# Performance work log

Measured on AMD Instinct MI355X. Metric: run time of the kernel, lower is better.

The kernel has to match this reference:

```python
import jax, jax.numpy as jnp
import numpy as np

B, T, H, D, V = 16, 64, 512, 512, 50257


def setup_inputs() -> dict:
    key = jax.random.key(0)
    ks = jax.random.split(key, 12)
    s = 0.05
    return {
        "sentiment_hidden": jax.random.normal(ks[0], (B, H), jnp.float32),
        "other_hidden": jax.random.normal(ks[1], (B, H), jnp.float32),
        "targets": jax.random.randint(ks[2], (B, T), 0, V),
        # SpaceTransformer: Linear(2H -> H) + ReLU (dropout inactive in eval)
        "Wc": jax.random.normal(ks[3], (H, 2 * H), jnp.float32) * s,
        "bc": jnp.zeros((H,), jnp.float32),
        # embedding table [V, D]
        "E": jax.random.normal(ks[4], (V, D), jnp.float32) * s,
        # LSTM params, PyTorch gate order (i, f, g, o)
        "W_ih": jax.random.normal(ks[5], (4 * H, D), jnp.float32) * s,
        "W_hh": jax.random.normal(ks[6], (4 * H, H), jnp.float32) * s,
        "b_ih": jnp.zeros((4 * H,), jnp.float32),
        "b_hh": jnp.zeros((4 * H,), jnp.float32),
        # output projection [V, H]
        "Wo": jax.random.normal(ks[7], (V, H), jnp.float32) * s,
        "bo": jnp.zeros((V,), jnp.float32),
    }


def reference(sentiment_hidden, other_hidden, targets, Wc, bc, E, W_ih, W_hh, b_ih, b_hh, Wo, bo):
    # combine: SpaceTransformer(Linear(2H->H) + ReLU)
    inputs = jax.nn.relu(jnp.concatenate([sentiment_hidden, other_hidden], axis=-1) @ Wc.T + bc)
    new_representation = inputs            # [B, H]
    bsz = inputs.shape[0]
    # teacher forcing: step 0 uses BOS token id 1, step t>0 uses targets[:, t-1]
    tokens = jnp.concatenate([jnp.ones((bsz, 1), targets.dtype), targets[:, :-1]], axis=1)  # [B, T]
    emb = E[tokens]                        # [B, T, D]
    # precompute input contribution to all gates: [B, T, 4H]
    xg = jnp.einsum("btd,gd->btg", emb, W_ih) + b_ih + b_hh

    def step(carry, x_t):                  # x_t: [B, 4H]
        h, c = carry
        g = x_t + h @ W_hh.T
        i, f, gg, o = jnp.split(g, 4, axis=-1)
        c = jax.nn.sigmoid(f) * c + jax.nn.sigmoid(i) * jnp.tanh(gg)
        h = jax.nn.sigmoid(o) * jnp.tanh(c)
        return (h, c), h

    c0 = jnp.zeros_like(inputs)
    (_, _), hs = jax.lax.scan(step, (inputs, c0), jnp.swapaxes(xg, 0, 1))
    hs = jnp.swapaxes(hs, 0, 1)            # [B, T, H]
    logits = jnp.einsum("bth,vh->btv", hs, Wo) + bo   # [B, T, V]
    predictions = jnp.argmax(logits, axis=-1)          # [B, T]
    return logits, predictions, new_representation
```

## Files before the change

kernel.cpp:

```cpp
#include <hip/hip_runtime.h>
#include <cstdint>
#include <cstddef>

typedef unsigned short u16;
typedef unsigned int   u32;
typedef unsigned long long u64;

typedef __attribute__((ext_vector_type(8))) short short8;
typedef __attribute__((ext_vector_type(4))) float f32x4;

#define NB_B 16
#define NT   64
#define NH   512
#define ND   512
#define NV   50257
#define NG   2048
#define LSTM_NBLK 32
#define UPB  16

__device__ __forceinline__ u16 f2bf(float f) {
    u32 u = __builtin_bit_cast(u32, f);
    return (u16)((u + 0x7FFFu + ((u >> 16) & 1u)) >> 16);
}
__device__ __forceinline__ float bf2f(u16 h) {
    return __builtin_bit_cast(float, (u32)h << 16);
}
__device__ __forceinline__ float sigm(float x) { return 1.0f / (1.0f + expf(-x)); }

__global__ void k_prep(const float* __restrict__ Whh, u16* __restrict__ Whi,
                       u16* __restrict__ Wlo, u64* __restrict__ argm,
                       u32* __restrict__ cnt) {
    int i = blockIdx.x * 256 + threadIdx.x;
    if (i < NG * NH) {
        float f = Whh[i];
        u16 hi = f2bf(f);
        Whi[i] = hi;
        Wlo[i] = f2bf(f - bf2f(hi));
    }
    if (i < NB_B * NT) argm[i] = 0ull;
    if (i < NT) cnt[i] = 0u;
}

__global__ __launch_bounds__(256) void k_combine(
    const float* __restrict__ sh, const float* __restrict__ oh,
    const float* __restrict__ Wc, const float* __restrict__ bc,
    float* __restrict__ h0, float* __restrict__ rep_out) {
    __shared__ float x[1024];
    int b = blockIdx.x, tid = threadIdx.x;
    for (int i = tid; i < 1024; i += 256)
        x[i] = (i < NH) ? sh[b * NH + i] : oh[b * NH + i - NH];
    __syncthreads();
    for (int n = tid; n < NH; n += 256) {
        const float* wr = Wc + (size_t)n * 1024;
        float s = 0.f;
        #pragma unroll 4
        for (int k = 0; k < 1024; k += 4) {
            float4 w = *(const float4*)(wr + k);
            s += x[k] * w.x + x[k+1] * w.y + x[k+2] * w.z + x[k+3] * w.w;
        }
        s += bc[n];
        s = fmaxf(s, 0.f);
        h0[b * NH + n] = s;
        rep_out[b * NH + n] = s;
    }
}

__global__ void k_gather(const int* __restrict__ targets, const float* __restrict__ E,
                         float* __restrict__ emb) {
    int bt = blockIdx.x;
    int b = bt >> 6, t = bt & 63;
    int tok = (t == 0) ? 1 : targets[b * NT + t - 1];
    const float4* s = (const float4*)(E + (size_t)tok * ND);
    float4* d = (float4*)(emb + (size_t)bt * ND);
    d[threadIdx.x] = s[threadIdx.x];
}

template<bool ARGMAX>
__global__ __launch_bounds__(256, 2) void k_gemm(
    const float* __restrict__ A,
    const float* __restrict__ Bm,
    const float* __restrict__ bias1,
    const float* __restrict__ bias2,
    float* __restrict__ C,
    u64* __restrict__ argm,
    int M, int N, int K, int NB) {
    __shared__ u16 sAh[128 * 64], sAl[128 * 64], sBh[128 * 64], sBl[128 * 64];
    int tid = threadIdx.x, lane = tid & 63, w = tid >> 6;
    int wm = w >> 1, wn = w & 1;

    int bid = blockIdx.x;
    int full = NB >> 3;
    int thresh = full << 6;
    int m_idx, n_idx;
    if (bid < thresh) {
        int g = bid >> 6, r = bid & 63;
        n_idx = g * 8 + (r & 7);
        m_idx = r >> 3;
    } else {
        int r2 = bid - thresh;
        int nrem = NB - (full << 3);
        n_idx = (full << 3) + r2 % nrem;
        m_idx = r2 / nrem;
    }
    int mbase = m_idx * 128, nbase = n_idx * 128;

    f32x4 acc[4][4];
    #pragma unroll
    for (int i = 0; i < 4; ++i)
        #pragma unroll
        for (int j = 0; j < 4; ++j) acc[i][j] = (f32x4){0.f, 0.f, 0.f, 0.f};

    const int lc = lane & 15, lk4 = lane >> 4;

    #pragma unroll 1
    for (int kc = 0; kc < K; kc += 64) {
        #pragma unroll
        for (int it = 0; it < 4; ++it) {
            int gi = tid + it * 256;
            int row = gi >> 3, gin = gi & 7;
            int gs8 = ((gin ^ (row & 7)) << 3);
            {
                const float* src = A + (size_t)(mbase + row) * K + kc + gin * 8;
                float4 f0 = *(const float4*)(src);
                float4 f1 = *(const float4*)(src + 4);
                float fv[8] = {f0.x, f0.y, f0.z, f0.w, f1.x, f1.y, f1.z, f1.w};
                short8 h8, l8;
                #pragma unroll
                for (int e = 0; e < 8; ++e) {
                    u16 hi = f2bf(fv[e]);
                    h8[e] = (short)hi;
                    l8[e] = (short)f2bf(fv[e] - bf2f(hi));
                }
                *(short8*)&sAh[row * 64 + gs8] = h8;
                *(short8*)&sAl[row * 64 + gs8] = l8;
            }
            {
                int n = nbase + row;
                short8 h8, l8;
                if (n < N) {
                    const float* src = Bm + (size_t)n * K + kc + gin * 8;
                    float4 f0 = *(const float4*)(src);
                    float4 f1 = *(const float4*)(src + 4);
                    float fv[8] = {f0.x, f0.y, f0.z, f0.w, f1.x, f1.y, f1.z, f1.w};
                    #pragma unroll
                    for (int e = 0; e < 8; ++e) {
                        u16 hi = f2bf(fv[e]);
                        h8[e] = (short)hi;
                        l8[e] = (short)f2bf(fv[e] - bf2f(hi));
                    }
                } else {
                    #pragma unroll
                    for (int e = 0; e < 8; ++e) { h8[e] = 0; l8[e] = 0; }
                }
                *(short8*)&sBh[row * 64 + gs8] = h8;
                *(short8*)&sBl[row * 64 + gs8] = l8;
            }
        }
        __syncthreads();
        #pragma unroll
        for (int ks = 0; ks < 2; ++ks) {
            short8 ah[4], al[4], bh[4], bl[4];
            #pragma unroll
            for (int mi = 0; mi < 4; ++mi) {
                int r = wm * 64 + mi * 16 + lc;
                int gs8 = (((ks * 4 + lk4) ^ (r & 7)) << 3);
                ah[mi] = *(const short8*)&sAh[r * 64 + gs8];
                al[mi] = *(const short8*)&sAl[r * 64 + gs8];
            }
            #pragma unroll
            for (int ni = 0; ni < 4; ++ni) {
                int r = wn * 64 + ni * 16 + lc;
                int gs8 = (((ks * 4 + lk4) ^ (r & 7)) << 3);
                bh[ni] = *(const short8*)&sBh[r * 64 + gs8];
                bl[ni] = *(const short8*)&sBl[r * 64 + gs8];
            }
            #pragma unroll
            for (int mi = 0; mi < 4; ++mi)
                #pragma unroll
                for (int ni = 0; ni < 4; ++ni) {
                    acc[mi][ni] = __builtin_amdgcn_mfma_f32_16x16x32_bf16(ah[mi], bh[ni], acc[mi][ni], 0, 0, 0);
                    acc[mi][ni] = __builtin_amdgcn_mfma_f32_16x16x32_bf16(al[mi], bh[ni], acc[mi][ni], 0, 0, 0);
                    acc[mi][ni] = __builtin_amdgcn_mfma_f32_16x16x32_bf16(ah[mi], bl[ni], acc[mi][ni], 0, 0, 0);
                }
        }
        __syncthreads();
    }

    float bsum[4];
    int cols[4];
    #pragma unroll
    for (int ni = 0; ni < 4; ++ni) {
        int col = nbase + wn * 64 + ni * 16 + lc;
        cols[ni] = col;
        float bv = 0.f;
        if (col < N) { bv = bias1[col]; if (bias2) bv += bias2[col]; }
        bsum[ni] = bv;
    }
    #pragma unroll
    for (int mi = 0; mi < 4; ++mi) {
        #pragma unroll
        for (int r_ = 0; r_ < 4; ++r_) {
            int row = mbase + wm * 64 + mi * 16 + (lk4 << 2) + r_;
            float* crow = C + (size_t)row * N;
            u64 best = 0ull;
            #pragma unroll
            for (int ni = 0; ni < 4; ++ni) {
                if (cols[ni] < N) {
                    float v = acc[mi][ni][r_] + bsum[ni];
                    crow[cols[ni]] = v;
                    if (ARGMAX) {
                        u32 bits = __builtin_bit_cast(u32, v);
                        u32 mono = (bits & 0x80000000u) ? ~bits : (bits | 0x80000000u);
                        u64 p = ((u64)mono << 32) | (u64)(0xFFFFFFFFu - (u32)cols[ni]);
                        best = best > p ? best : p;
                    }
                }
            }
            if (ARGMAX) {
                #pragma unroll
                for (int s = 1; s < 16; s <<= 1) {
                    u64 o = __shfl_xor((unsigned long long)best, s, 64);
                    best = best > o ? best : o;
                }
                if (lc == 0) atomicMax(&argm[row], best);
            }
        }
    }
}

__global__ __launch_bounds__(256, 1) void k_lstm(
    const float* __restrict__ xg, const float* __restrict__ h0,
    const u16* __restrict__ Whi, const u16* __restrict__ Wlo,
    float* __restrict__ hs,
    u32* __restrict__ Ghi, u32* __restrict__ Glo,
    u32* __restrict__ cnt) {
    __shared__ u16 hhi[16 * 512];
    __shared__ u16 hlo[16 * 512];
    __shared__ float g_lds[4 * 256];

    const int tid = threadIdx.x;
    const int lane = tid & 63, w = tid >> 6;
    const int blk = blockIdx.x;
    const int u0 = blk * UPB;
    const int lc = lane & 15, lk4 = lane >> 4;
    const int bown = tid >> 4, uown = tid & 15;

    short8 bh[16], bl[16];
    {
        size_t base = (size_t)(w * NH + u0 + lc) * NH + lk4 * 8;
        #pragma unroll
        for (int kk = 0; kk < 16; ++kk) {
            bh[kk] = *(const short8*)(Whi + base + kk * 32);
            bl[kk] = *(const short8*)(Wlo + base + kk * 32);
        }
    }

    #pragma unroll
    for (int i = 0; i < 32; ++i) {
        int idx = i * 256 + tid;
        int b = idx >> 9, k = idx & 511;
        float f = h0[b * NH + k];
        u16 hi = f2bf(f), lo = f2bf(f - bf2f(hi));
        int g = k >> 3;
        int ea = b * 512 + ((g ^ (b & 7)) << 3) + (k & 7);
        hhi[ea] = hi;
        hlo[ea] = lo;
    }
    float c = 0.f;
    __syncthreads();

    #pragma unroll 1
    for (int t = 0; t < NT; ++t) {
        f32x4 a0 = (f32x4){0.f,0.f,0.f,0.f};
        f32x4 a1 = (f32x4){0.f,0.f,0.f,0.f};
        f32x4 a2 = (f32x4){0.f,0.f,0.f,0.f};
        #pragma unroll
        for (int kk = 0; kk < 16; ++kk) {
            int g = kk * 4 + lk4;
            int ea = lc * 512 + ((g ^ (lc & 7)) << 3);
            short8 ah = *(const short8*)&hhi[ea];
            short8 al = *(const short8*)&hlo[ea];
            a0 = __builtin_amdgcn_mfma_f32_16x16x32_bf16(ah, bh[kk], a0, 0, 0, 0);
            a1 = __builtin_amdgcn_mfma_f32_16x16x32_bf16(al, bh[kk], a1, 0, 0, 0);
            a2 = __builtin_amdgcn_mfma_f32_16x16x32_bf16(ah, bl[kk], a2, 0, 0, 0);
        }
        #pragma unroll
        for (int r = 0; r < 4; ++r)
            g_lds[w * 256 + (lk4 * 4 + r) * 16 + lc] = a0[r] + a1[r] + a2[r];
        __syncthreads();

        const float* xrow = xg + (size_t)(bown * NT + t) * NG + u0 + uown;
        float gi = g_lds[0 * 256 + tid] + xrow[0];
        float gf = g_lds[1 * 256 + tid] + xrow[NH];
        float gg = g_lds[2 * 256 + tid] + xrow[2 * NH];
        float go = g_lds[3 * 256 + tid] + xrow[3 * NH];
        c = sigm(gf) * c + sigm(gi) * tanhf(gg);
        float h = sigm(go) * tanhf(c);
        hs[(size_t)(bown * NT + t) * NH + u0 + uown] = h;

        if (t < NT - 1) {
            u16 hi = f2bf(h), lo = f2bf(h - bf2f(hi));
            u32 ohi = (u32)(u16)__shfl_xor((int)(u32)hi, 1, 64);
            u32 olo = (u32)(u16)__shfl_xor((int)(u32)lo, 1, 64);
            int buf = (t & 1) * 4096;
            if ((tid & 1) == 0) {
                int word = bown * 256 + ((u0 + uown) >> 1);
                __hip_atomic_store(&Ghi[buf + word], (u32)hi | (ohi << 16),
                                   __ATOMIC_RELAXED, __HIP_MEMORY_SCOPE_AGENT);
                __hip_atomic_store(&Glo[buf + word], (u32)lo | (olo << 16),
                                   __ATOMIC_RELAXED, __HIP_MEMORY_SCOPE_AGENT);
            }
            __threadfence();
            __syncthreads();
            if (tid == 0) {
                __hip_atomic_fetch_add(&cnt[t], 1u, __ATOMIC_RELEASE, __HIP_MEMORY_SCOPE_AGENT);
                while (__hip_atomic_load(&cnt[t], __ATOMIC_ACQUIRE, __HIP_MEMORY_SCOPE_AGENT) < LSTM_NBLK) {}
            }
            __syncthreads();
            #pragma unroll
            for (int i = 0; i < 16; ++i) {
                int word = i * 256 + tid;
                int b = word >> 8, k2 = word & 255;
                u32 vh = __hip_atomic_load(&Ghi[buf + word], __ATOMIC_RELAXED, __HIP_MEMORY_SCOPE_AGENT);
                u32 vl = __hip_atomic_load(&Glo[buf + word], __ATOMIC_RELAXED, __HIP_MEMORY_SCOPE_AGENT);
                int k = k2 * 2, g = k >> 3;
                int ea = b * 512 + ((g ^ (b & 7)) << 3) + (k & 7);
                *(u32*)&hhi[ea] = vh;
                *(u32*)&hlo[ea] = vl;
            }
            __syncthreads();
        }
    }
}

__global__ void k_decode(const u64* __restrict__ argm, float* __restrict__ pred) {
    int i = blockIdx.x * 256 + threadIdx.x;
    if (i < NB_B * NT) {
        u32 enc = (u32)(argm[i] & 0xFFFFFFFFull);
        pred[i] = (float)(0xFFFFFFFFu - enc);
    }
}

extern "C" void kernel_launch(void* const* d_in, const int* in_sizes, int n_in,
                              void* d_out, int out_size, void* d_ws, size_t ws_size,
                              hipStream_t stream) {
    const float* sh  = (const float*)d_in[0];
    const float* oh  = (const float*)d_in[1];
    const int*   tg  = (const int*)d_in[2];
    const float* Wc  = (const float*)d_in[3];
    const float* bc  = (const float*)d_in[4];
    const float* E   = (const float*)d_in[5];
    const float* Wih = (const float*)d_in[6];
    const float* Whh = (const float*)d_in[7];
    const float* bih = (const float*)d_in[8];
    const float* bhh = (const float*)d_in[9];
    const float* Wo  = (const float*)d_in[10];
    const float* bo  = (const float*)d_in[11];

    float* out_logits = (float*)d_out;
    float* out_pred   = out_logits + (size_t)NB_B * NT * NV;
    float* out_rep    = out_pred + NB_B * NT;

    char* ws = (char*)d_ws;
    u16*   Whi  = (u16*)(ws);
    u16*   Wlo  = (u16*)(ws + (size_t)2  * 1024 * 1024);
    float* emb  = (float*)(ws + (size_t)4  * 1024 * 1024);
    float* xg   = (float*)(ws + (size_t)6  * 1024 * 1024);
    float* hs   = (float*)(ws + (size_t)14 * 1024 * 1024);
    float* h0   = (float*)(ws + (size_t)16 * 1024 * 1024);
    u64*   argm = (u64*)(ws + (size_t)16 * 1024 * 1024 + 32 * 1024);
    u32*   Ghi  = (u32*)(ws + (size_t)16 * 1024 * 1024 + 40 * 1024);
    u32*   Glo  = (u32*)(ws + (size_t)16 * 1024 * 1024 + 72 * 1024);
    u32*   cnt  = (u32*)(ws + (size_t)16 * 1024 * 1024 + 104 * 1024);

    k_prep<<<dim3(4096), dim3(256), 0, stream>>>(Whh, Whi, Wlo, argm, cnt);
    k_combine<<<dim3(NB_B), dim3(256), 0, stream>>>(sh, oh, Wc, bc, h0, out_rep);
    k_gather<<<dim3(NB_B * NT), dim3(128), 0, stream>>>(tg, E, emb);
    k_gemm<false><<<dim3(8 * 16), dim3(256), 0, stream>>>(
        emb, Wih, bih, bhh, xg, (u64*)nullptr, NB_B * NT, NG, ND, 16);
    k_lstm<<<dim3(LSTM_NBLK), dim3(256), 0, stream>>>(xg, h0, Whi, Wlo, hs, Ghi, Glo, cnt);
    k_gemm<true><<<dim3(8 * 393), dim3(256), 0, stream>>>(
        hs, Wo, bo, (const float*)nullptr, out_logits, argm, NB_B * NT, NV, NH, 393);
    k_decode<<<dim3(4), dim3(256), 0, stream>>>(argm, out_pred);
}
```

Baseline: 1.396 ms.

## Pre-pack Wo and hs as bf16 hi/lo pairs; per-block flag barrier in LSTM

Adds a packing pass that converts Wo once into interleaved bf16 hi/lo u32 words, so the logits GEMM tiles no longer re-split fp32 into bf16 pairs on every load (Wo is reloaded for each of the eight M tiles). The LSTM now writes packed hidden states directly, which the output GEMM consumes without conversion. The LSTM step barrier changes from a shared atomic counter with a spin by thread 0 to per-block flags polled by 32 lanes with sleep, and the hidden-state exchange uses a packed layout. The packed Wo buffer needs about 100 MB of workspace and an extra pass over Wo. The new barrier drops the explicit release fence and relies on vmcnt waits, so memory ordering is a risk.

```diff
diff --git a/kernel.cpp b/kernel.cpp
--- a/kernel.cpp
+++ b/kernel.cpp
@@ -1,4 +1,5 @@
 #include <hip/hip_runtime.h>
+#include <hip/hip_bf16.h>
 #include <cstdint>
 #include <cstddef>
 
@@ -19,8 +20,8 @@
 #define UPB  16
 
 __device__ __forceinline__ u16 f2bf(float f) {
-    u32 u = __builtin_bit_cast(u32, f);
-    return (u16)((u + 0x7FFFu + ((u >> 16) & 1u)) >> 16);
+    __hip_bfloat16 b = __float2bfloat16(f);
+    return __builtin_bit_cast(u16, b);
 }
 __device__ __forceinline__ float bf2f(u16 h) {
     return __builtin_bit_cast(float, (u32)h << 16);
@@ -29,7 +30,7 @@
 
 __global__ void k_prep(const float* __restrict__ Whh, u16* __restrict__ Whi,
                        u16* __restrict__ Wlo, u64* __restrict__ argm,
-                       u32* __restrict__ cnt) {
+                       u32* __restrict__ flags) {
     int i = blockIdx.x * 256 + threadIdx.x;
     if (i < NG * NH) {
         float f = Whh[i];
@@ -38,7 +39,24 @@
         Wlo[i] = f2bf(f - bf2f(hi));
     }
     if (i < NB_B * NT) argm[i] = 0ull;
-    if (i < NT) cnt[i] = 0u;
+    if (i < NT * LSTM_NBLK) flags[i] = 0u;
+}
+
+__global__ void k_pack_wo(const float* __restrict__ Wo, u32* __restrict__ Wo_pk) {
+    size_t base = ((size_t)blockIdx.x * 256 + threadIdx.x) * 8;
+    if (base >= (size_t)NV * NH) return;
+    float4 f0 = *(const float4*)(Wo + base);
+    float4 f1 = *(const float4*)(Wo + base + 4);
+    float fv[8] = {f0.x, f0.y, f0.z, f0.w, f1.x, f1.y, f1.z, f1.w};
+    u32 ov[8];
+    #pragma unroll
+    for (int e = 0; e < 8; ++e) {
+        u16 hi = f2bf(fv[e]);
+        u16 lo = f2bf(fv[e] - bf2f(hi));
+        ov[e] = ((u32)hi << 16) | (u32)lo;
+    }
+    *(uint4*)(Wo_pk + base) = (uint4){ov[0], ov[1], ov[2], ov[3]};
+    *(uint4*)(Wo_pk + base + 4) = (uint4){ov[4], ov[5], ov[6], ov[7]};
 }
 
 __global__ __launch_bounds__(256) void k_combine(
@@ -75,10 +93,10 @@
     d[threadIdx.x] = s[threadIdx.x];
 }
 
-template<bool ARGMAX>
+template<bool ARGMAX, bool APK, bool BPK>
 __global__ __launch_bounds__(256, 2) void k_gemm(
-    const float* __restrict__ A,
-    const float* __restrict__ Bm,
+    const void* __restrict__ Av,
+    const void* __restrict__ Bv,
     const float* __restrict__ bias1,
     const float* __restrict__ bias2,
     float* __restrict__ C,
@@ -120,25 +138,19 @@
             int row = gi >> 3, gin = gi & 7;
             int gs8 = ((gin ^ (row & 7)) << 3);
             {
-                const float* src = A + (size_t)(mbase + row) * K + kc + gin * 8;
-                float4 f0 = *(const float4*)(src);
-                float4 f1 = *(const float4*)(src + 4);
-                float fv[8] = {f0.x, f0.y, f0.z, f0.w, f1.x, f1.y, f1.z, f1.w};
                 short8 h8, l8;
-                #pragma unroll
-                for (int e = 0; e < 8; ++e) {
-                    u16 hi = f2bf(fv[e]);
-                    h8[e] = (short)hi;
-                    l8[e] = (short)f2bf(fv[e] - bf2f(hi));
-                }
-                *(short8*)&sAh[row * 64 + gs8] = h8;
-                *(short8*)&sAl[row * 64 + gs8] = l8;
-            }
-            {
-                int n = nbase + row;
-                short8 h8, l8;
-                if (n < N) {
-                    const float* src = Bm + (size_t)n * K + kc + gin * 8;
+                if (APK) {
+                    const u32* src = (const u32*)Av + (size_t)(mbase + row) * K + kc + gin * 8;
+                    uint4 p0 = *(const uint4*)(src);
+                    uint4 p1 = *(const uint4*)(src + 4);
+                    u32 pv[8] = {p0.x, p0.y, p0.z, p0.w, p1.x, p1.y, p1.z, p1.w};
+                    #pragma unroll
+                    for (int e = 0; e < 8; ++e) {
+                        h8[e] = (short)(u16)(pv[e] >> 16);
+                        l8[e] = (short)(u16)(pv[e] & 0xFFFFu);
+                    }
+                } else {
+                    const float* src = (const float*)Av + (size_t)(mbase + row) * K + kc + gin * 8;
                     float4 f0 = *(const float4*)(src);
                     float4 f1 = *(const float4*)(src + 4);
                     float fv[8] = {f0.x, f0.y, f0.z, f0.w, f1.x, f1.y, f1.z, f1.w};
@@ -147,6 +159,36 @@
                         u16 hi = f2bf(fv[e]);
                         h8[e] = (short)hi;
                         l8[e] = (short)f2bf(fv[e] - bf2f(hi));
+                    }
+                }
+                *(short8*)&sAh[row * 64 + gs8] = h8;
+                *(short8*)&sAl[row * 64 + gs8] = l8;
+            }
+            {
+                int n = nbase + row;
+                short8 h8, l8;
+                if (n < N) {
+                    if (BPK) {
+                        const u32* src = (const u32*)Bv + (size_t)n * K + kc + gin * 8;
+                        uint4 p0 = *(const uint4*)(src);
+                        uint4 p1 = *(const uint4*)(src + 4);
+                        u32 pv[8] = {p0.x, p0.y, p0.z, p0.w, p1.x, p1.y, p1.z, p1.w};
+                        #pragma unroll
+                        for (int e = 0; e < 8; ++e) {
+                            h8[e] = (short)(u16)(pv[e] >> 16);
+                            l8[e] = (short)(u16)(pv[e] & 0xFFFFu);
+                        }
+                    } else {
+                        const float* src = (const float*)Bv + (size_t)n * K + kc + gin * 8;
+                        float4 f0 = *(const float4*)(src);
+                        float4 f1 = *(const float4*)(src + 4);
+                        float fv[8] = {f0.x, f0.y, f0.z, f0.w, f1.x, f1.y, f1.z, f1.w};
+                        #pragma unroll
+                        for (int e = 0; e < 8; ++e) {
+                            u16 hi = f2bf(fv[e]);
+                            h8[e] = (short)hi;
+                            l8[e] = (short)f2bf(fv[e] - bf2f(hi));
+                        }
                     }
                 } else {
                     #pragma unroll
@@ -231,9 +273,9 @@
 __global__ __launch_bounds__(256, 1) void k_lstm(
     const float* __restrict__ xg, const float* __restrict__ h0,
     const u16* __restrict__ Whi, const u16* __restrict__ Wlo,
-    float* __restrict__ hs,
-    u32* __restrict__ Ghi, u32* __restrict__ Glo,
-    u32* __restrict__ cnt) {
+    u32* __restrict__ hs_pk,
+    u32* __restrict__ H,
+    u32* __restrict__ flags) {
     __shared__ u16 hhi[16 * 512];
     __shared__ u16 hlo[16 * 512];
     __shared__ float g_lds[4 * 256];
@@ -296,37 +338,42 @@
         float go = g_lds[3 * 256 + tid] + xrow[3 * NH];
         c = sigm(gf) * c + sigm(gi) * tanhf(gg);
         float h = sigm(go) * tanhf(c);
-        hs[(size_t)(bown * NT + t) * NH + u0 + uown] = h;
+        u16 hi = f2bf(h), lo = f2bf(h - bf2f(hi));
+        u32 pk = ((u32)hi << 16) | (u32)lo;
+        hs_pk[(size_t)(bown * NT + t) * NH + u0 + uown] = pk;
 
         if (t < NT - 1) {
-            u16 hi = f2bf(h), lo = f2bf(h - bf2f(hi));
-            u32 ohi = (u32)(u16)__shfl_xor((int)(u32)hi, 1, 64);
-            u32 olo = (u32)(u16)__shfl_xor((int)(u32)lo, 1, 64);
-            int buf = (t & 1) * 4096;
-            if ((tid & 1) == 0) {
-                int word = bown * 256 + ((u0 + uown) >> 1);
-                __hip_atomic_store(&Ghi[buf + word], (u32)hi | (ohi << 16),
+            const int buf = (t & 1) * 8192;
+            __hip_atomic_store(&H[buf + bown * NH + u0 + uown], pk,
+                               __ATOMIC_RELAXED, __HIP_MEMORY_SCOPE_AGENT);
+            asm volatile("s_waitcnt vmcnt(0)" ::: "memory");
+            __syncthreads();
+            if (tid == 0)
+                __hip_atomic_store(&flags[t * LSTM_NBLK + blk], 1u,
                                    __ATOMIC_RELAXED, __HIP_MEMORY_SCOPE_AGENT);
-                __hip_atomic_store(&Glo[buf + word], (u32)lo | (olo << 16),
-                                   __ATOMIC_RELAXED, __HIP_MEMORY_SCOPE_AGENT);
-            }
-            __threadfence();
-            __syncthreads();
-            if (tid == 0) {
-                __hip_atomic_fetch_add(&cnt[t], 1u, __ATOMIC_RELEASE, __HIP_MEMORY_SCOPE_AGENT);
-                while (__hip_atomic_load(&cnt[t], __ATOMIC_ACQUIRE, __HIP_MEMORY_SCOPE_AGENT) < LSTM_NBLK) {}
-            }
-            __syncthreads();
+            if (lane < LSTM_NBLK) {
+                while (__hip_atomic_load(&flags[t * LSTM_NBLK + lane],
+                                         __ATOMIC_RELAXED, __HIP_MEMORY_SCOPE_AGENT) == 0) {
+                    __builtin_amdgcn_s_sleep(1);
+                }
+            }
+            asm volatile("" ::: "memory");
             #pragma unroll
-            for (int i = 0; i < 16; ++i) {
-                int word = i * 256 + tid;
-                int b = word >> 8, k2 = word & 255;
-                u32 vh = __hip_atomic_load(&Ghi[buf + word], __ATOMIC_RELAXED, __HIP_MEMORY_SCOPE_AGENT);
-                u32 vl = __hip_atomic_load(&Glo[buf + word], __ATOMIC_RELAXED, __HIP_MEMORY_SCOPE_AGENT);
-                int k = k2 * 2, g = k >> 3;
-                int ea = b * 512 + ((g ^ (b & 7)) << 3) + (k & 7);
-                *(u32*)&hhi[ea] = vh;
-                *(u32*)&hlo[ea] = vl;
+            for (int i = 0; i < 4; ++i) {
+                int grp = i * 256 + tid;
+                int b = grp >> 6, gidx = grp & 63;
+                int ubase = gidx << 3;
+                short8 h8, l8;
+                #pragma unroll
+                for (int e = 0; e < 8; ++e) {
+                    u32 v = __hip_atomic_load(&H[buf + b * NH + ubase + e],
+                                              __ATOMIC_RELAXED, __HIP_MEMORY_SCOPE_AGENT);
+                    h8[e] = (short)(u16)(v >> 16);
+                    l8[e] = (short)(u16)(v & 0xFFFFu);
+                }
+                int ea = b * 512 + ((gidx ^ (b & 7)) << 3);
+                *(short8*)&hhi[ea] = h8;
+                *(short8*)&hlo[ea] = l8;
             }
             __syncthreads();
         }
@@ -362,24 +409,32 @@
     float* out_rep    = out_pred + NB_B * NT;
 
     char* ws = (char*)d_ws;
-    u16*   Whi  = (u16*)(ws);
-    u16*   Wlo  = (u16*)(ws + (size_t)2  * 1024 * 1024);
-    float* emb  = (float*)(ws + (size_t)4  * 1024 * 1024);
-    float* xg   = (float*)(ws + (size_t)6  * 1024 * 1024);
-    float* hs   = (float*)(ws + (size_t)14 * 1024 * 1024);
-    float* h0   = (float*)(ws + (size_t)16 * 1024 * 1024);
-    u64*   argm = (u64*)(ws + (size_t)16 * 1024 * 1024 + 32 * 1024);
-    u32*   Ghi  = (u32*)(ws + (size_t)16 * 1024 * 1024 + 40 * 1024);
-    u32*   Glo  = (u32*)(ws + (size_t)16 * 1024 * 1024 + 72 * 1024);
-    u32*   cnt  = (u32*)(ws + (size_t)16 * 1024 * 1024 + 104 * 1024);
-
-    k_prep<<<dim3(4096), dim3(256), 0, stream>>>(Whh, Whi, Wlo, argm, cnt);
+    u16*   Whi   = (u16*)(ws);
+    u16*   Wlo   = (u16*)(ws + (size_t)2  * 1024 * 1024);
+    float* emb   = (float*)(ws + (size_t)4  * 1024 * 1024);
+    float* xg    = (float*)(ws + (size_t)6  * 1024 * 1024);
+    u32*   hs_pk = (u32*)(ws + (size_t)14 * 1024 * 1024);
+    float* h0    = (float*)(ws + (size_t)16 * 1024 * 1024);
+    u64*   argm  = (u64*)(ws + (size_t)16 * 1024 * 1024 + 32 * 1024);
+    u32*   H     = (u32*)(ws + (size_t)16 * 1024 * 1024 + 40 * 1024);
+    u32*   flags = (u32*)(ws + (size_t)16 * 1024 * 1024 + 104 * 1024);
+    size_t wo_off = (size_t)16 * 1024 * 1024 + 112 * 1024;
+    u32*   Wo_pk = (u32*)(ws + wo_off);
+    const bool use_bpk = ws_size >= wo_off + (size_t)NV * NH * sizeof(u32);
+
+    k_prep<<<dim3(4096), dim3(256), 0, stream>>>(Whh, Whi, Wlo, argm, flags);
     k_combine<<<dim3(NB_B), dim3(256), 0, stream>>>(sh, oh, Wc, bc, h0, out_rep);
     k_gather<<<dim3(NB_B * NT), dim3(128), 0, stream>>>(tg, E, emb);
-    k_gemm<false><<<dim3(8 * 16), dim3(256), 0, stream>>>(
+    k_gemm<false, false, false><<<dim3(8 * 16), dim3(256), 0, stream>>>(
         emb, Wih, bih, bhh, xg, (u64*)nullptr, NB_B * NT, NG, ND, 16);
-    k_lstm<<<dim3(LSTM_NBLK), dim3(256), 0, stream>>>(xg, h0, Whi, Wlo, hs, Ghi, Glo, cnt);
-    k_gemm<true><<<dim3(8 * 393), dim3(256), 0, stream>>>(
-        hs, Wo, bo, (const float*)nullptr, out_logits, argm, NB_B * NT, NV, NH, 393);
+    if (use_bpk)
+        k_pack_wo<<<dim3(12565), dim3(256), 0, stream>>>(Wo, Wo_pk);
+    k_lstm<<<dim3(LSTM_NBLK), dim3(256), 0, stream>>>(xg, h0, Whi, Wlo, hs_pk, H, flags);
+    if (use_bpk)
+        k_gemm<true, true, true><<<dim3(8 * 393), dim3(256), 0, stream>>>(
+            hs_pk, Wo_pk, bo, (const float*)nullptr, out_logits, argm, NB_B * NT, NV, NH, 393);
+    else
+        k_gemm<true, true, false><<<dim3(8 * 393), dim3(256), 0, stream>>>(
+            hs_pk, Wo, bo, (const float*)nullptr, out_logits, argm, NB_B * NT, NV, NH, 393);
     k_decode<<<dim3(4), dim3(256), 0, stream>>>(argm, out_pred);
 }
```

New measurement: 1.220 ms. 12.6% less time.
